# Kernel optimization log

Measured on AMD Instinct MI355X. Metric: run time of the kernel, lower is better.

Reference implementation:

```python
import jax, jax.numpy as jnp
import numpy as np

B, T, CIN, HID, OUT, H, W = 8, 8, 128, 64, 64, 32, 32


def _conv(x, w, b):
    # x: [B, C, H, W], w: [O, C, kh, kw] -> SAME-padded conv, stride 1
    y = jax.lax.conv_general_dilated(x, w, (1, 1), "SAME",
                                     dimension_numbers=("NCHW", "OIHW", "NCHW"))
    return y + b[None, :, None, None]


def _layer_dir(xs, w_ih, w_hh, b_ih, b_hh, reverse):
    # xs: [T, B, C, H, W]; one direction of a ConvLSTM layer; returns hs [T, B, HID, H, W]
    b, hh_, ww_ = xs.shape[1], xs.shape[3], xs.shape[4]
    h0 = jnp.zeros((b, HID, hh_, ww_), xs.dtype)

    def step(carry, x):
        h, c = carry
        gates = _conv(x, w_ih, b_ih) + _conv(h, w_hh, b_hh)  # [B, 4*HID, H, W]
        i, f, g, o = jnp.split(gates, 4, axis=1)
        c = jax.nn.sigmoid(f) * c + jax.nn.sigmoid(i) * jnp.tanh(g)
        h = jax.nn.sigmoid(o) * jnp.tanh(c)
        return (h, c), h

    _, hs = jax.lax.scan(step, (h0, h0), xs, reverse=reverse)
    return hs


def _forward(features, w_ih0f, w_hh0f, b_ih0f, b_hh0f,
             w_ih0r, w_hh0r, b_ih0r, b_hh0r,
             w_ih1f, w_hh1f, b_ih1f, b_hh1f,
             w_ih1r, w_hh1r, b_ih1r, b_hh1r,
             w_out, b_out):
    xs = jnp.transpose(features, (1, 0, 2, 3, 4))  # [T, B, C, H, W]
    # layer 0, both directions (scan reverse=True aligns outputs to original time order)
    hf = _layer_dir(xs, w_ih0f, w_hh0f, b_ih0f, b_hh0f, False)
    hr = _layer_dir(xs, w_ih0r, w_hh0r, b_ih0r, b_hh0r, True)
    xs1 = jnp.concatenate([hf, hr], axis=2)  # [T, B, 2*HID, H, W] (dropout is identity at eval)
    # layer 1
    hf1 = _layer_dir(xs1, w_ih1f, w_hh1f, b_ih1f, b_hh1f, False)
    hr1 = _layer_dir(xs1, w_ih1r, w_hh1r, b_ih1r, b_hh1r, True)
    last = jnp.concatenate([hf1[-1], hr1[-1]], axis=1)  # output[:, -1] -> [B, 2*HID, H, W]
    return jax.nn.relu(_conv(last, w_out, b_out))


def setup_inputs() -> dict:
    key = jax.random.key(0)
    ks = jax.random.split(key, 24)
    G = 4 * HID
    p = lambda k, s: jax.random.normal(k, s, jnp.float32) * 0.05
    d = {"features": jax.random.normal(ks[0], (B, T, CIN, H, W), jnp.float32)}
    i = 1
    for l, cin in ((0, CIN), (1, 2 * HID)):
        for dr in ("f", "r"):
            d[f"w_ih{l}{dr}"] = p(ks[i], (G, cin, 3, 3)); i += 1
            d[f"w_hh{l}{dr}"] = p(ks[i], (G, HID, 3, 3)); i += 1
            d[f"b_ih{l}{dr}"] = p(ks[i], (G,)); i += 1
            d[f"b_hh{l}{dr}"] = p(ks[i], (G,)); i += 1
    d["w_out"] = p(ks[i], (OUT, 2 * HID, 1, 1)); i += 1
    d["b_out"] = p(ks[i], (OUT,))
    return d


def reference(features, w_ih0f, w_hh0f, b_ih0f, b_hh0f,
              w_ih0r, w_hh0r, b_ih0r, b_hh0r,
              w_ih1f, w_hh1f, b_ih1f, b_hh1f,
              w_ih1r, w_hh1r, b_ih1r, b_hh1r,
              w_out, b_out):
    return _forward(features, w_ih0f, w_hh0f, b_ih0f, b_hh0f,
                    w_ih0r, w_hh0r, b_ih0r, b_hh0r,
                    w_ih1f, w_hh1f, b_ih1f, b_hh1f,
                    w_ih1r, w_hh1r, b_ih1r, b_hh1r,
                    w_out, b_out)
```

## Files before the change

### kernel.cpp

```cpp
#include <hip/hip_runtime.h>
#include <math.h>
#include <stdint.h>


typedef __attribute__((ext_vector_type(8))) short short8;
typedef __attribute__((ext_vector_type(4))) float float4v;

namespace {
constexpr int IMG = 34 * 34 * 64;
constexpr size_t SLOTI = 16ull * IMG;
constexpr int ROWB = 34 * 128;
constexpr int PADB = 8192;
}
template <int N> struct IC { static constexpr int v = N; };

__device__ __forceinline__ uint16_t bf16_rne(float x) {
  uint32_t u = __builtin_bit_cast(uint32_t, x);
  return (uint16_t)((u + 0x7FFFu + ((u >> 16) & 1u)) >> 16);
}
__device__ __forceinline__ float bf16_to_f(uint16_t h) {
  uint32_t u = ((uint32_t)h) << 16;
  return __builtin_bit_cast(float, u);
}

__device__ __forceinline__ void gl_lds16(const void* g, void* l) {
  __builtin_amdgcn_global_load_lds(
      (const __attribute__((address_space(1))) void*)g,
      (__attribute__((address_space(3))) void*)l, 16, 0, 0);
}

__global__ void pack_features(const float* __restrict__ f, uint16_t* __restrict__ out) {
  const size_t i = (size_t)blockIdx.x * 256 + threadIdx.x;
  const int blk_s = (int)(i & 7);
  size_t pp = i >> 3;
  const int px = (int)(pp % 34); pp /= 34;
  const int yy = (int)(pp % 34); pp /= 34;
  const int cg = (int)(pp & 3);
  const int bt = (int)(pp >> 2);
  const int b = bt & 7, t = bt >> 3;
  const int blk = blk_s ^ (px & 7);
  const int pl = blk >> 2, kg = blk & 3;
  short8 sv;
  if (px == 0 || px == 33 || yy == 0 || yy == 33) {
    #pragma unroll
    for (int j = 0; j < 8; ++j) sv[j] = 0;
  } else {
    const int x = px - 1, y = yy - 1;
    #pragma unroll
    for (int j = 0; j < 8; ++j) {
      const int ch = cg * 32 + kg * 8 + j;
      const float fv = f[(((size_t)b * 8 + t) * 128 + ch) * 1024 + y * 32 + x];
      const uint16_t hi = bf16_rne(fv);
      sv[j] = (short)(pl ? bf16_rne(fv - bf16_to_f(hi)) : hi);
    }
  }
  *(short8*)(out + i * 8) = sv;
}

struct WPackArgs {
  const float* wih[4]; const float* whh[4];
  const float* bih[4]; const float* bhh[4];
  uint32_t* wp; float* bp;
};
__global__ void pack_weights(WPackArgs A) {
  const int combo = blockIdx.y;
  const int idx = blockIdx.x * 256 + threadIdx.x;
  const int q = idx & 4095;
  const int rest = idx >> 12;
  const int nt = rest & 1;
  const int ct = rest >> 1;
  const int tap = ct % 9, cg = ct / 9;
  const int w2 = q & 3;
  const int b8s = (q >> 2) & 7;
  const int hcp = (q >> 5) & 15;
  const int g = (q >> 9) & 3;
  const int pl = (q >> 11) & 1;
  const int b8 = b8s ^ (hcp & 7);
  const int kg = b8 & 3;
  const int hcl = hcp * 2 + (b8 >> 2);
  const int n = g * 64 + nt * 32 + hcl;
  const float* wih = A.wih[combo];
  const float* whh = A.whh[combo];
  uint32_t out = 0;
  #pragma unroll
  for (int e = 0; e < 2; ++e) {
    const int ch = cg * 32 + kg * 8 + w2 * 2 + e;
    const float wv = (ch < 128) ? wih[((size_t)n * 128 + ch) * 9 + tap]
                                : whh[((size_t)n * 64 + (ch - 128)) * 9 + tap];
    const uint16_t hi = bf16_rne(wv);
    const uint16_t v = pl ? bf16_rne(wv - bf16_to_f(hi)) : hi;
    out |= ((uint32_t)v) << (16 * e);
  }
  A.wp[(size_t)combo * 442368 + idx] = out;
  if (idx < 256) A.bp[combo * 256 + idx] = A.bih[combo][idx] + A.bhh[combo][idx];
}

struct StepArgs {
  const uint16_t* in0; const uint16_t* in1; const uint16_t* in2;
  int nc0, nc1, nc2;
  const uint32_t* W;
  const float* bias;
  float* cbuf;
  uint16_t* himg;
  float* hf32;
};

template <int ROWS, int NW>
__global__ __launch_bounds__(NW * 64, 1) void conv_lstm_step(StepArgs A0, StepArgs A1) {
  constexpr int THREADS = NW * 64;
  constexpr int BANDS = 32 / ROWS;
  constexpr int BSH = (ROWS == 8) ? 2 : 3;
  constexpr int ABYTES = (ROWS + 2) * ROWB;
  constexpr int ACH = (ABYTES + NW * 1024 - 1) / (NW * 1024);
  constexpr int ASLOT = ACH * NW * 1024;
  constexpr int WCH = 8 / NW;
  constexpr int CNT0 = WCH;
  constexpr int CNT12 = WCH + ACH;

  extern __shared__ char smem[];
  char* Asm_ = smem;
  char* Wsm_ = smem + 2 * ASLOT;

  const StepArgs a = (blockIdx.z == 0) ? A0 : A1;
  const int bx = blockIdx.x;
  const int Q4 = bx & 3;
  const int band = (bx >> 2) & (BANDS - 1);
  const int b = bx >> (2 + BSH);
  const int nt = Q4 >> 1;
  const int nq = Q4 & 1;
  const int y0 = band * ROWS;
  const int tid = threadIdx.x;
  const int lane = tid & 63;
  const int w = tid >> 6;
  const int m15 = lane & 15;
  const int kg = lane >> 4;

  int offA[2][2][3][2];
  #pragma unroll
  for (int row = 0; row < 2; ++row)
    #pragma unroll
    for (int xh = 0; xh < 2; ++xh)
      #pragma unroll
      for (int kx = 0; kx < 3; ++kx)
        #pragma unroll
        for (int pl = 0; pl < 2; ++pl) {
          const int px = xh * 16 + kx + m15;
          const int sw = (pl * 4 + kg) ^ (px & 7);
          offA[row][xh][kx][pl] = (2 * w + row) * ROWB + px * 128 + sw * 16;
        }
  int offW[2][4];
  {
    const int hcpl = m15 >> 1;
    const int b8 = kg + 4 * (m15 & 1);
    #pragma unroll
    for (int pl = 0; pl < 2; ++pl)
      #pragma unroll
      for (int g = 0; g < 4; ++g)
        offW[pl][g] = (((pl * 4 + g) * 8 + hcpl) * 8 + (b8 ^ hcpl)) * 16;
  }

  const int ncg = a.nc0 + a.nc1 + a.nc2;
  auto abase = [&](int cg) -> const char* {
    const uint16_t* t;
    if (cg < a.nc0) t = a.in0 + ((size_t)b * a.nc0 + cg) * IMG;
    else if (cg < a.nc0 + a.nc1) t = a.in1 + ((size_t)b * a.nc1 + (cg - a.nc0)) * IMG;
    else t = a.in2 + ((size_t)b * a.nc2 + (cg - a.nc0 - a.nc1)) * IMG;
    return (const char*)t + (size_t)y0 * ROWB;
  };
  auto stageA = [&](int cgi, int par) {
    const char* g = abase(cgi);
    char* d = Asm_ + par * ASLOT;
    #pragma unroll
    for (int j = 0; j < ACH; ++j)
      gl_lds16(g + (size_t)(ACH * w + j) * 1024 + lane * 16, d + (ACH * w + j) * 1024);
  };
  auto stageW = [&](int cgs, int taps, int slot) {
    const char* g = (const char*)a.W + ((size_t)((cgs * 9 + taps) * 2 + nt) << 14)
                  + (size_t)nq * 1024;
    char* d = Wsm_ + slot * 8192;
    #pragma unroll
    for (int j = 0; j < WCH; ++j) {
      const int c = WCH * w + j;
      gl_lds16(g + (size_t)c * 2048 + lane * 16, d + c * 1024);
    }
  };

  float4v acc[2][2][4];
  #pragma unroll
  for (int row = 0; row < 2; ++row)
    #pragma unroll
    for (int xh = 0; xh < 2; ++xh)
      #pragma unroll
      for (int g = 0; g < 4; ++g) acc[row][xh][g] = (float4v){0.f, 0.f, 0.f, 0.f};

  stageA(0, 0);
  stageW(0, 0, 0);
  stageW(0, 1, 1);

  for (int cg = 0; cg < ncg; ++cg) {
    auto tap_body = [&](auto tapc) {
      constexpr int TAP = decltype(tapc)::v;
      constexpr int CNT = (TAP == 1 || TAP == 2) ? CNT12 : CNT0;
      asm volatile("s_waitcnt vmcnt(%0)\n\ts_barrier" :: "n"(CNT) : "memory");
      const int lin = cg * 9 + TAP;
      {
        const int l2 = lin + 2;
        int cgs = l2 / 9;
        const int taps = l2 % 9;
        if (cgs >= ncg) cgs = 0;
        stageW(cgs, taps, l2 % 3);
      }
      if (TAP == 0) {
        const int nx = (cg + 1 < ncg) ? cg + 1 : 0;
        stageA(nx, (cg + 1) & 1);
      }
      constexpr int ky = TAP / 3, kx = TAP % 3;
      const char* Ab = Asm_ + (cg & 1) * ASLOT + ky * ROWB;
      const char* Wb = Wsm_ + (lin % 3) * 8192;
      short8 af[2][2][2];
      #pragma unroll
      for (int row = 0; row < 2; ++row)
        #pragma unroll
        for (int xh = 0; xh < 2; ++xh)
          #pragma unroll
          for (int pl = 0; pl < 2; ++pl)
            af[row][xh][pl] = *(const short8*)(Ab + offA[row][xh][kx][pl]);
      short8 wfr[2][4];
      #pragma unroll
      for (int pl = 0; pl < 2; ++pl)
        #pragma unroll
        for (int g = 0; g < 4; ++g)
          wfr[pl][g] = *(const short8*)(Wb + offW[pl][g]);
      #pragma unroll
      for (int row = 0; row < 2; ++row)
        #pragma unroll
        for (int xh = 0; xh < 2; ++xh)
          #pragma unroll
          for (int g = 0; g < 4; ++g) {
            acc[row][xh][g] = __builtin_amdgcn_mfma_f32_16x16x32_bf16(af[row][xh][0], wfr[0][g], acc[row][xh][g], 0, 0, 0);
            acc[row][xh][g] = __builtin_amdgcn_mfma_f32_16x16x32_bf16(af[row][xh][0], wfr[1][g], acc[row][xh][g], 0, 0, 0);
            acc[row][xh][g] = __builtin_amdgcn_mfma_f32_16x16x32_bf16(af[row][xh][1], wfr[0][g], acc[row][xh][g], 0, 0, 0);
          }
    };
    tap_body(IC<0>{}); tap_body(IC<1>{}); tap_body(IC<2>{});
    tap_body(IC<3>{}); tap_body(IC<4>{}); tap_body(IC<5>{});
    tap_body(IC<6>{}); tap_body(IC<7>{}); tap_body(IC<8>{});
  }
  asm volatile("s_waitcnt vmcnt(0)" ::: "memory");

  const int hc = Q4 * 16 + m15;
  float bi[4];
  #pragma unroll
  for (int g = 0; g < 4; ++g) bi[g] = a.bias[g * 64 + hc];
  const int img = Q4 >> 1;
  const int chi = (Q4 & 1) * 16 + m15;
  const int kgb = chi >> 3, jj = chi & 7;
  uint16_t* hb = a.himg ? a.himg + ((size_t)(b * 2 + img)) * IMG : nullptr;
  #pragma unroll
  for (int row = 0; row < 2; ++row) {
    const int y = y0 + 2 * w + row;
    float* crow = a.cbuf + ((size_t)(b * 64 + hc)) * 1024 + y * 32;
    float* hrow = a.hf32 ? a.hf32 + ((size_t)(b * 64 + hc)) * 1024 + y * 32 : nullptr;
    #pragma unroll
    for (int xh = 0; xh < 2; ++xh) {
      const int x0 = xh * 16 + kg * 4;
      float4v cv = *(float4v*)(crow + x0);
      float4v cn, hn;
      #pragma unroll
      for (int q = 0; q < 4; ++q) {
        const float ig = 1.f / (1.f + expf(-(acc[row][xh][0][q] + bi[0])));
        const float fg = 1.f / (1.f + expf(-(acc[row][xh][1][q] + bi[1])));
        const float gg = tanhf(acc[row][xh][2][q] + bi[2]);
        const float og = 1.f / (1.f + expf(-(acc[row][xh][3][q] + bi[3])));
        const float c2 = fg * cv[q] + ig * gg;
        cn[q] = c2;
        hn[q] = og * tanhf(c2);
      }
      *(float4v*)(crow + x0) = cn;
      if (hrow) *(float4v*)(hrow + x0) = hn;
      if (hb) {
        #pragma unroll
        for (int q = 0; q < 4; ++q) {
          const int px = x0 + q + 1;
          const int sw = px & 7;
          const uint16_t hi = bf16_rne(hn[q]);
          const uint16_t lo = bf16_rne(hn[q] - bf16_to_f(hi));
          const size_t p16 = ((size_t)(y + 1) * 34 + px) * 64;
          hb[p16 + (size_t)(kgb ^ sw) * 8 + jj] = hi;
          hb[p16 + (size_t)((4 + kgb) ^ sw) * 8 + jj] = lo;
        }
      }
    }
  }
  if (hb) {
    for (int i = tid; i < ROWS * 128; i += THREADS) {
      const int rr = i >> 7;
      const int hlf = (i >> 6) & 1;
      const int jx = i & 63;
      hb[((size_t)(y0 + 1 + rr) * 34 + hlf * 33) * 64 + jx] = 0;
    }
    if (band == 0) for (int i = tid; i < 2176; i += THREADS) hb[i] = 0;
    if (band == BANDS - 1) for (int i = tid; i < 2176; i += THREADS) hb[(size_t)33 * 2176 + i] = 0;
  }
}

__global__ void final_conv(const float* __restrict__ h1f_last, const float* __restrict__ h1r_last,
                           const float* __restrict__ wout, const float* __restrict__ bout,
                           float* __restrict__ out) {
  __shared__ float Ws[16 * 128];
  const int oq = blockIdx.y;
  for (int i = threadIdx.x; i < 16 * 128; i += 256) Ws[i] = wout[oq * 16 * 128 + i];
  __syncthreads();
  const int gp = blockIdx.x * 256 + threadIdx.x;
  const int b = gp >> 10, p = gp & 1023;
  float acc[16];
  #pragma unroll
  for (int o = 0; o < 16; ++o) acc[o] = bout[oq * 16 + o];
  for (int c = 0; c < 128; ++c) {
    const float xv = (c < 64) ? h1f_last[((size_t)b * 64 + c) * 1024 + p]
                              : h1r_last[((size_t)b * 64 + (c - 64)) * 1024 + p];
    #pragma unroll
    for (int o = 0; o < 16; ++o) acc[o] = fmaf(xv, Ws[o * 128 + c], acc[o]);
  }
  #pragma unroll
  for (int o = 0; o < 16; ++o) {
    const float v = acc[o];
    out[((size_t)b * 64 + oq * 16 + o) * 1024 + p] = v > 0.f ? v : 0.f;
  }
}

extern "C" void kernel_launch(void* const* d_in, const int* in_sizes, int n_in,
                              void* d_out, int out_size, void* d_ws, size_t ws_size,
                              hipStream_t stream) {
  char* p = (char*)d_ws;
  uint16_t* featImg = (uint16_t*)p; p += (size_t)8 * 8 * 4 * IMG * 2 + PADB;
  uint32_t* WP = (uint32_t*)p;      p += (size_t)4 * 442368 * 4;
  float* bp = (float*)p;            p += 4096;
  uint16_t* hf0i = (uint16_t*)p;    p += (size_t)9 * SLOTI * 2 + PADB;
  uint16_t* hr0i = (uint16_t*)p;    p += (size_t)9 * SLOTI * 2 + PADB;
  uint16_t* h1fi = (uint16_t*)p;    p += (size_t)2 * SLOTI * 2 + PADB;
  float* c0f = (float*)p;           p += (size_t)4 * 2097152;
  float* c0r = c0f + 524288;
  float* c1f = c0r + 524288;
  float* c1r = c1f + 524288;
  float* h1f8 = (float*)p;          p += 2097152;
  float* h1r8 = (float*)p;          p += 2097152;

  hipMemsetAsync(c0f, 0, (size_t)4 * 2097152, stream);
  hipMemsetAsync(hf0i, 0, (size_t)SLOTI * 2, stream);
  hipMemsetAsync(hr0i + (size_t)8 * SLOTI, 0, (size_t)SLOTI * 2, stream);
  hipMemsetAsync(h1fi, 0, (size_t)SLOTI * 2, stream);

  pack_features<<<dim3(9248), 256, 0, stream>>>((const float*)d_in[0], featImg);

  WPackArgs wa;
  for (int combo = 0; combo < 4; ++combo) {
    const int base = 1 + combo * 4;
    wa.wih[combo] = (const float*)d_in[base];
    wa.whh[combo] = (const float*)d_in[base + 1];
    wa.bih[combo] = (const float*)d_in[base + 2];
    wa.bhh[combo] = (const float*)d_in[base + 3];
  }
  wa.wp = WP; wa.bp = bp;
  pack_weights<<<dim3(1728, 4), 256, 0, stream>>>(wa);

  constexpr int DYN_P = 2 * 45056 + 3 * 8192;
  constexpr int DYN_S = 2 * 26624 + 3 * 8192;
  (void)hipFuncSetAttribute((const void*)(conv_lstm_step<8, 4>),
                            hipFuncAttributeMaxDynamicSharedMemorySize, DYN_P);
  (void)hipFuncSetAttribute((const void*)(conv_lstm_step<4, 2>),
                            hipFuncAttributeMaxDynamicSharedMemorySize, DYN_S);

  auto mk = [&](const uint16_t* i0, int n0, const uint16_t* i1, int n1,
                const uint16_t* i2, int n2, int combo, float* cb,
                uint16_t* himg, float* hf32) {
    StepArgs s;
    s.in0 = i0; s.in1 = i1; s.in2 = i2;
    s.nc0 = n0; s.nc1 = n1; s.nc2 = n2;
    s.W = WP + (size_t)combo * 442368; s.bias = bp + combo * 256;
    s.cbuf = cb; s.himg = himg; s.hf32 = hf32;
    return s;
  };

  for (int k = 0; k < 8; ++k) {
    const int tr = 7 - k;
    StepArgs f = mk(featImg + (size_t)k * 8 * 4 * IMG, 4,
                    hf0i + (size_t)k * SLOTI, 2, nullptr, 0,
                    0, c0f, hf0i + (size_t)(k + 1) * SLOTI, nullptr);
    StepArgs r = mk(featImg + (size_t)tr * 8 * 4 * IMG, 4,
                    hr0i + (size_t)(tr + 1) * SLOTI, 2, nullptr, 0,
                    1, c0r, hr0i + (size_t)tr * SLOTI, nullptr);
    conv_lstm_step<8, 4><<<dim3(128, 1, 2), 256, DYN_P, stream>>>(f, r);
  }

  for (int t = 0; t < 8; ++t) {
    uint16_t* himg = (t < 7) ? h1fi + (size_t)((t + 1) & 1) * SLOTI : nullptr;
    float* hf32 = (t == 7) ? h1f8 : nullptr;
    StepArgs s = mk(hf0i + (size_t)(t + 1) * SLOTI, 2, hr0i + (size_t)t * SLOTI, 2,
                    h1fi + (size_t)(t & 1) * SLOTI, 2, 2, c1f, himg, hf32);
    if (t == 0) {
      StepArgs rv = mk(hf0i + (size_t)8 * SLOTI, 2, hr0i + (size_t)7 * SLOTI, 2,
                       nullptr, 0, 3, c1r, nullptr, h1r8);
      conv_lstm_step<8, 4><<<dim3(128, 1, 2), 256, DYN_P, stream>>>(s, rv);
    } else {
      conv_lstm_step<4, 2><<<dim3(256, 1, 1), 128, DYN_S, stream>>>(s, s);
    }
  }

  final_conv<<<dim3(32, 4), 256, 0, stream>>>(
      h1f8, h1r8, (const float*)d_in[17], (const float*)d_in[18], (float*)d_out);
}
```

Before: 811.6 us.

## Shrink row bands and retile waves to double grid size and occupancy

```diff
diff --git a/kernel.cpp b/kernel.cpp
--- a/kernel.cpp
+++ b/kernel.cpp
@@ -105,15 +105,16 @@
   float* hf32;
 };
 
-template <int ROWS, int NW>
-__global__ __launch_bounds__(NW * 64, 1) void conv_lstm_step(StepArgs A0, StepArgs A1) {
+template <int ROWS, int NW, int MT>
+__global__ __launch_bounds__(NW * 64, 2) void conv_lstm_step(StepArgs A0, StepArgs A1) {
+  static_assert(NW * MT == ROWS * 2, "wave tiling must cover the band");
   constexpr int THREADS = NW * 64;
   constexpr int BANDS = 32 / ROWS;
-  constexpr int BSH = (ROWS == 8) ? 2 : 3;
+  constexpr int BSH = (ROWS == 4) ? 3 : 4;
   constexpr int ABYTES = (ROWS + 2) * ROWB;
   constexpr int ACH = (ABYTES + NW * 1024 - 1) / (NW * 1024);
   constexpr int ASLOT = ACH * NW * 1024;
-  constexpr int WCH = 8 / NW;
+  constexpr int WCH = 8192 / (NW * 1024);
   constexpr int CNT0 = WCH;
   constexpr int CNT12 = WCH + ACH;
 
@@ -135,19 +136,20 @@
   const int m15 = lane & 15;
   const int kg = lane >> 4;
 
-  int offA[2][2][3][2];
-  #pragma unroll
-  for (int row = 0; row < 2; ++row)
-    #pragma unroll
-    for (int xh = 0; xh < 2; ++xh)
-      #pragma unroll
-      for (int kx = 0; kx < 3; ++kx)
-        #pragma unroll
-        for (int pl = 0; pl < 2; ++pl) {
-          const int px = xh * 16 + kx + m15;
-          const int sw = (pl * 4 + kg) ^ (px & 7);
-          offA[row][xh][kx][pl] = (2 * w + row) * ROWB + px * 128 + sw * 16;
-        }
+  int offA[MT][3][2];
+  #pragma unroll
+  for (int m = 0; m < MT; ++m) {
+    const int mt = w * MT + m;
+    const int row = mt >> 1, xh = mt & 1;
+    #pragma unroll
+    for (int kx = 0; kx < 3; ++kx)
+      #pragma unroll
+      for (int pl = 0; pl < 2; ++pl) {
+        const int px = xh * 16 + kx + m15;
+        const int sw = (pl * 4 + kg) ^ (px & 7);
+        offA[m][kx][pl] = row * ROWB + px * 128 + sw * 16;
+      }
+  }
   int offW[2][4];
   {
     const int hcpl = m15 >> 1;
@@ -185,13 +187,11 @@
     }
   };
 
-  float4v acc[2][2][4];
-  #pragma unroll
-  for (int row = 0; row < 2; ++row)
-    #pragma unroll
-    for (int xh = 0; xh < 2; ++xh)
-      #pragma unroll
-      for (int g = 0; g < 4; ++g) acc[row][xh][g] = (float4v){0.f, 0.f, 0.f, 0.f};
+  float4v acc[MT][4];
+  #pragma unroll
+  for (int m = 0; m < MT; ++m)
+    #pragma unroll
+    for (int g = 0; g < 4; ++g) acc[m][g] = (float4v){0.f, 0.f, 0.f, 0.f};
 
   stageA(0, 0);
   stageW(0, 0, 0);
@@ -217,14 +217,12 @@
       constexpr int ky = TAP / 3, kx = TAP % 3;
       const char* Ab = Asm_ + (cg & 1) * ASLOT + ky * ROWB;
       const char* Wb = Wsm_ + (lin % 3) * 8192;
-      short8 af[2][2][2];
-      #pragma unroll
-      for (int row = 0; row < 2; ++row)
+      short8 af[MT][2];
+      #pragma unroll
+      for (int m = 0; m < MT; ++m)
         #pragma unroll
-        for (int xh = 0; xh < 2; ++xh)
-          #pragma unroll
-          for (int pl = 0; pl < 2; ++pl)
-            af[row][xh][pl] = *(const short8*)(Ab + offA[row][xh][kx][pl]);
+        for (int pl = 0; pl < 2; ++pl)
+          af[m][pl] = *(const short8*)(Ab + offA[m][kx][pl]);
       short8 wfr[2][4];
       #pragma unroll
       for (int pl = 0; pl < 2; ++pl)
@@ -232,15 +230,13 @@
         for (int g = 0; g < 4; ++g)
           wfr[pl][g] = *(const short8*)(Wb + offW[pl][g]);
       #pragma unroll
-      for (int row = 0; row < 2; ++row)
+      for (int m = 0; m < MT; ++m)
         #pragma unroll
-        for (int xh = 0; xh < 2; ++xh)
-          #pragma unroll
-          for (int g = 0; g < 4; ++g) {
-            acc[row][xh][g] = __builtin_amdgcn_mfma_f32_16x16x32_bf16(af[row][xh][0], wfr[0][g], acc[row][xh][g], 0, 0, 0);
-            acc[row][xh][g] = __builtin_amdgcn_mfma_f32_16x16x32_bf16(af[row][xh][0], wfr[1][g], acc[row][xh][g], 0, 0, 0);
-            acc[row][xh][g] = __builtin_amdgcn_mfma_f32_16x16x32_bf16(af[row][xh][1], wfr[0][g], acc[row][xh][g], 0, 0, 0);
-          }
+        for (int g = 0; g < 4; ++g) {
+          acc[m][g] = __builtin_amdgcn_mfma_f32_16x16x32_bf16(af[m][0], wfr[0][g], acc[m][g], 0, 0, 0);
+          acc[m][g] = __builtin_amdgcn_mfma_f32_16x16x32_bf16(af[m][0], wfr[1][g], acc[m][g], 0, 0, 0);
+          acc[m][g] = __builtin_amdgcn_mfma_f32_16x16x32_bf16(af[m][1], wfr[0][g], acc[m][g], 0, 0, 0);
+        }
     };
     tap_body(IC<0>{}); tap_body(IC<1>{}); tap_body(IC<2>{});
     tap_body(IC<3>{}); tap_body(IC<4>{}); tap_body(IC<5>{});
@@ -257,38 +253,36 @@
   const int kgb = chi >> 3, jj = chi & 7;
   uint16_t* hb = a.himg ? a.himg + ((size_t)(b * 2 + img)) * IMG : nullptr;
   #pragma unroll
-  for (int row = 0; row < 2; ++row) {
-    const int y = y0 + 2 * w + row;
+  for (int m = 0; m < MT; ++m) {
+    const int mt = w * MT + m;
+    const int y = y0 + (mt >> 1);
+    const int x0 = (mt & 1) * 16 + kg * 4;
     float* crow = a.cbuf + ((size_t)(b * 64 + hc)) * 1024 + y * 32;
     float* hrow = a.hf32 ? a.hf32 + ((size_t)(b * 64 + hc)) * 1024 + y * 32 : nullptr;
-    #pragma unroll
-    for (int xh = 0; xh < 2; ++xh) {
-      const int x0 = xh * 16 + kg * 4;
-      float4v cv = *(float4v*)(crow + x0);
-      float4v cn, hn;
+    float4v cv = *(float4v*)(crow + x0);
+    float4v cn, hn;
+    #pragma unroll
+    for (int q = 0; q < 4; ++q) {
+      const float ig = 1.f / (1.f + expf(-(acc[m][0][q] + bi[0])));
+      const float fg = 1.f / (1.f + expf(-(acc[m][1][q] + bi[1])));
+      const float gg = tanhf(acc[m][2][q] + bi[2]);
+      const float og = 1.f / (1.f + expf(-(acc[m][3][q] + bi[3])));
+      const float c2 = fg * cv[q] + ig * gg;
+      cn[q] = c2;
+      hn[q] = og * tanhf(c2);
+    }
+    *(float4v*)(crow + x0) = cn;
+    if (hrow) *(float4v*)(hrow + x0) = hn;
+    if (hb) {
       #pragma unroll
       for (int q = 0; q < 4; ++q) {
-        const float ig = 1.f / (1.f + expf(-(acc[row][xh][0][q] + bi[0])));
-        const float fg = 1.f / (1.f + expf(-(acc[row][xh][1][q] + bi[1])));
-        const float gg = tanhf(acc[row][xh][2][q] + bi[2]);
-        const float og = 1.f / (1.f + expf(-(acc[row][xh][3][q] + bi[3])));
-        const float c2 = fg * cv[q] + ig * gg;
-        cn[q] = c2;
-        hn[q] = og * tanhf(c2);
-      }
-      *(float4v*)(crow + x0) = cn;
-      if (hrow) *(float4v*)(hrow + x0) = hn;
-      if (hb) {
-        #pragma unroll
-        for (int q = 0; q < 4; ++q) {
-          const int px = x0 + q + 1;
-          const int sw = px & 7;
-          const uint16_t hi = bf16_rne(hn[q]);
-          const uint16_t lo = bf16_rne(hn[q] - bf16_to_f(hi));
-          const size_t p16 = ((size_t)(y + 1) * 34 + px) * 64;
-          hb[p16 + (size_t)(kgb ^ sw) * 8 + jj] = hi;
-          hb[p16 + (size_t)((4 + kgb) ^ sw) * 8 + jj] = lo;
-        }
+        const int px = x0 + q + 1;
+        const int sw = px & 7;
+        const uint16_t hi = bf16_rne(hn[q]);
+        const uint16_t lo = bf16_rne(hn[q] - bf16_to_f(hi));
+        const size_t p16 = ((size_t)(y + 1) * 34 + px) * 64;
+        hb[p16 + (size_t)(kgb ^ sw) * 8 + jj] = hi;
+        hb[p16 + (size_t)((4 + kgb) ^ sw) * 8 + jj] = lo;
       }
     }
   }
@@ -364,11 +358,11 @@
   wa.wp = WP; wa.bp = bp;
   pack_weights<<<dim3(1728, 4), 256, 0, stream>>>(wa);
 
-  constexpr int DYN_P = 2 * 45056 + 3 * 8192;
-  constexpr int DYN_S = 2 * 26624 + 3 * 8192;
-  (void)hipFuncSetAttribute((const void*)(conv_lstm_step<8, 4>),
+  constexpr int DYN_P = 2 * 28672 + 3 * 8192;
+  constexpr int DYN_S = 2 * 20480 + 3 * 8192;
+  (void)hipFuncSetAttribute((const void*)(conv_lstm_step<4, 4, 2>),
                             hipFuncAttributeMaxDynamicSharedMemorySize, DYN_P);
-  (void)hipFuncSetAttribute((const void*)(conv_lstm_step<4, 2>),
+  (void)hipFuncSetAttribute((const void*)(conv_lstm_step<2, 4, 1>),
                             hipFuncAttributeMaxDynamicSharedMemorySize, DYN_S);
 
   auto mk = [&](const uint16_t* i0, int n0, const uint16_t* i1, int n1,
@@ -390,7 +384,7 @@
     StepArgs r = mk(featImg + (size_t)tr * 8 * 4 * IMG, 4,
                     hr0i + (size_t)(tr + 1) * SLOTI, 2, nullptr, 0,
                     1, c0r, hr0i + (size_t)tr * SLOTI, nullptr);
-    conv_lstm_step<8, 4><<<dim3(128, 1, 2), 256, DYN_P, stream>>>(f, r);
+    conv_lstm_step<4, 4, 2><<<dim3(256, 1, 2), 256, DYN_P, stream>>>(f, r);
   }
 
   for (int t = 0; t < 8; ++t) {
@@ -401,9 +395,9 @@
     if (t == 0) {
       StepArgs rv = mk(hf0i + (size_t)8 * SLOTI, 2, hr0i + (size_t)7 * SLOTI, 2,
                        nullptr, 0, 3, c1r, nullptr, h1r8);
-      conv_lstm_step<8, 4><<<dim3(128, 1, 2), 256, DYN_P, stream>>>(s, rv);
+      conv_lstm_step<4, 4, 2><<<dim3(256, 1, 2), 256, DYN_P, stream>>>(s, rv);
     } else {
-      conv_lstm_step<4, 2><<<dim3(256, 1, 1), 128, DYN_S, stream>>>(s, s);
+      conv_lstm_step<2, 4, 1><<<dim3(512, 1, 1), 256, DYN_S, stream>>>(s, s);
     }
   }
 
```

Result: faster. 742.8 us (-8.5%).
